# Kernel tuning notes

Hardware: AMD Instinct MI355X
Metric: run time of the kernel (lower is better)

## Reference

```python
import jax, jax.numpy as jnp
import numpy as np

B, D, L = 16, 256, 200
T = 1000   # max_frame_length
K = 3      # kernel_size
DW, DC = 4, 2


def setup_inputs() -> dict:
    key = jax.random.key(0)
    ks = jax.random.split(key, 16)
    plen = jax.random.randint(ks[0], (B,), 150, L + 1)
    pm = jnp.arange(L)[None, :] < plen[:, None]              # (B,L) True=valid
    phoneme_mask = pm[:, None, :]                            # (B,1,L)
    durations = jax.random.uniform(ks[1], (B, L), minval=1.0, maxval=8.0) * pm
    phoneme = jax.random.normal(ks[2], (B, D, L), dtype=jnp.float32)
    s = 0.05
    params = {
        'Wpw': jax.random.normal(ks[3], (D, D)) * s, 'bpw': jnp.zeros((D,)),
        'Cw': jax.random.normal(ks[4], (8, D, K)) * s, 'cbw': jnp.zeros((8,)),
        'Mw': jax.random.normal(ks[5], (10, DW)) * s, 'mbw': jnp.zeros((DW,)),
        'Lw': jax.random.normal(ks[6], (DW * D, D)) * s, 'lbw': jnp.zeros((D,)),
        'Wpc': jax.random.normal(ks[7], (D, D)) * s, 'bpc': jnp.zeros((D,)),
        'Cc': jax.random.normal(ks[8], (8, D, K)) * s, 'cbc': jnp.zeros((8,)),
        'Mc': jax.random.normal(ks[9], (10, DC)) * s, 'mbc': jnp.zeros((DC,)),
        'Lc': jax.random.normal(ks[10], (DW * DC, D)) * s, 'lbc': jnp.zeros((D,)),
        'Wo': jax.random.normal(ks[11], (D, 2 * D)) * s, 'bo': jnp.zeros((2 * D,)),
    }
    return {'durations': durations, 'phoneme': phoneme, 'phoneme_mask': phoneme_mask, **params}


def _conv_swish(x, W1, b1, Ck, cb, pm):
    # 1x1 conv (proj) then kernel-K 'same' conv then SiLU; mask padded phones
    h = jnp.einsum('od,bdl->bol', W1, x) + b1[None, :, None]
    h = jax.lax.conv_general_dilated(h, Ck, (1,), 'SAME',
                                     dimension_numbers=('NCH', 'OIH', 'NCH')) + cb[None, :, None]
    h = jax.nn.silu(h)
    h = jnp.where(pm[:, None, :], h, 0.0)
    return h.transpose(0, 2, 1)  # (B, L, 8)


def _mlp(S, E, h, M, mb):
    # concat start/end boundary scalars with per-phone conv features -> (B,T,L,10)
    feat = jnp.concatenate([S[..., None], E[..., None],
                            jnp.broadcast_to(h[:, None], (B, T, L, 8))], axis=-1)
    return jax.nn.silu(feat @ M + mb)


def _forward(durations, phoneme, phoneme_mask, Wpw, bpw, Cw, cbw, Mw, mbw, Lw, lbw,
             Wpc, bpc, Cc, cbc, Mc, mbc, Lc, lbc, Wo, bo):
    pm = phoneme_mask[:, 0, :]                                          # (B,L)
    frame_lengths = jnp.clip(jnp.round(durations.sum(-1)).astype(jnp.int32), 0, T)
    frame_mask = jnp.arange(T)[None, :] < frame_lengths[:, None]        # (B,T)
    attn_mask = frame_mask[:, :, None] & pm[:, None, :]                 # (B,T,L)
    sd = jnp.cumsum(durations, axis=-1)                                 # (B,L)
    sk = sd - durations
    t = jnp.arange(1, T + 1, dtype=durations.dtype)
    S = jnp.where(attn_mask, t[None, :, None] - sk[:, None, :], 0.0)    # (B,T,L)
    E = jnp.where(attn_mask, (sd - sk)[:, None, :], 0.0)                # (B,T,L)

    h_w = _conv_swish(phoneme, Wpw, bpw, Cw, cbw, pm)
    w = _mlp(S, E, h_w, Mw, mbw)                                        # (B,T,L,DW)
    w = jnp.where(pm[:, None, :, None], w, -jnp.inf)
    w = jax.nn.softmax(w, axis=2)                                       # softmax over phones
    w = jnp.where(frame_mask[:, :, None, None], w, 0.0)

    h_c = _conv_swish(phoneme, Wpc, bpc, Cc, cbc, pm)
    c = _mlp(S, E, h_c, Mc, mbc)                                        # (B,T,L,DC)

    wh = jnp.einsum('btlq,bdl->btqd', w, phoneme).reshape(B, T, DW * D) @ Lw + lbw
    wc = jnp.einsum('btlq,btlp->btqp', w, c).reshape(B, T, DW * DC) @ Lc + lbc
    whc = jnp.where(frame_mask[..., None], wh + wc, 0.0)                # (B,T,D)
    out = (whc @ Wo + bo).transpose(0, 2, 1)                            # (B,2D,T)
    return out, frame_mask, frame_lengths, w.transpose(0, 3, 1, 2)


def reference(durations, phoneme, phoneme_mask, Wpw, bpw, Cw, cbw, Mw, mbw, Lw, lbw,
              Wpc, bpc, Cc, cbc, Mc, mbc, Lc, lbc, Wo, bo):
    out, frame_mask, frame_lengths, w = _forward(
        durations, phoneme, phoneme_mask, Wpw, bpw, Cw, cbw, Mw, mbw, Lw, lbw,
        Wpc, bpc, Cc, cbc, Mc, mbc, Lc, lbc, Wo, bo)
    mean, log_std = jnp.split(out, 2, axis=1)                           # (B,D,T) each
    return (mean, log_std, frame_mask, frame_lengths, w)
```

## Files before the change

kernel.cpp:

```cpp
#include <hip/hip_runtime.h>
#include <hip/hip_bf16.h>
#include <math.h>

#define NB 16
#define ND 256
#define NL 200
#define NT 1000

typedef unsigned short ushort_t;
typedef __bf16 bf16x8 __attribute__((ext_vector_type(8)));
typedef float f32x4 __attribute__((ext_vector_type(4)));

#define OFF_PHT   0u
#define OFF_SK    4966400u
#define OFF_EW    4969600u
#define OFF_EC    4975744u
#define OFF_BW2   4981888u
#define OFF_BC2   4981912u
#define OFF_FL    4981936u
#define OFF_GT    11535552u
#define OFF_WOT   15221952u
#define OFF_BASE  15287488u
#define OFF_PHTB  15320256u
#define OFF_LWT   15844544u

__device__ __forceinline__ float silu_f(float x){ return x / (1.f + __expf(-x)); }
__device__ __forceinline__ ushort_t f2bf(float x){
  __hip_bfloat16 h = __float2bfloat16(x);
  return *(ushort_t*)&h;
}

__global__ __launch_bounds__(256) void k_stage1(
    const float* __restrict__ dur, const float* __restrict__ ph,
    const float* __restrict__ Wp_w, const float* __restrict__ C_w, const float* __restrict__ bp_w,
    const float* __restrict__ Wp_c, const float* __restrict__ C_c, const float* __restrict__ bp_c,
    const float* __restrict__ Wo, const float* __restrict__ Lw,
    float* __restrict__ sk_ws, int* __restrict__ fl_ws,
    float* __restrict__ o_fm, float* __restrict__ o_fl,
    float* __restrict__ Ew, float* __restrict__ Ec,
    float* __restrict__ bw2, float* __restrict__ bc2,
    ushort_t* __restrict__ WoT, ushort_t* __restrict__ LwT,
    float* __restrict__ phT, ushort_t* __restrict__ phTb)
{
  int bid = blockIdx.x, tid = threadIdx.x;
  if (bid < 16){
    int b = bid;
    __shared__ float sdur[NL];
    __shared__ float ssk[NL];
    __shared__ int sfl;
    if (tid < NL) sdur[tid] = dur[b*NL + tid];
    __syncthreads();
    if (tid == 0){
      float run = 0.f;
      for (int l = 0; l < NL; ++l){ ssk[l] = run; run += sdur[l]; }
      int fl = (int)rintf(run);
      fl = fl < 0 ? 0 : (fl > NT ? NT : fl);
      sfl = fl; fl_ws[b] = fl; o_fl[b] = (float)fl;
    }
    __syncthreads();
    if (tid < NL) sk_ws[b*NL + tid] = ssk[tid];
    for (int t = tid; t < NT; t += 256) o_fm[b*NT + t] = (t < sfl) ? 1.f : 0.f;
  } else if (bid < 1600){
    int sbid = bid - 16;
    if (sbid < 48){
      int gid = sbid*256 + tid;
      int branch = gid / 6144;
      int r = gid % 6144;
      int d = r & 255;
      int ock = r >> 8;
      int oc = ock / 3, k = ock % 3;
      const float* Wp = branch ? Wp_c : Wp_w;
      const float* C  = branch ? C_c  : C_w;
      float acc = 0.f;
      for (int i = 0; i < ND; ++i) acc += C[(oc*ND + i)*3 + k] * Wp[i*ND + d];
      (branch ? Ec : Ew)[r] = acc;
      if (d == 0){
        const float* bp = branch ? bp_c : bp_w;
        float bb = 0.f;
        for (int i = 0; i < ND; ++i) bb += C[(oc*ND + i)*3 + k] * bp[i];
        (branch ? bc2 : bw2)[ock] = bb;
      }
    } else {
      int gid = (sbid - 48)*256 + tid;
      if (gid < 131072){
        int n = gid >> 8, k = gid & 255;
        WoT[gid] = f2bf(Wo[(size_t)k*512 + n]);
      } else {
        int r = gid - 131072;
        int d = r & 255;
        int qn = r >> 8;
        int q = qn >> 8, n = qn & 255;
        LwT[r] = f2bf(Lw[((size_t)q*256 + d)*256 + n]);
      }
    }
  } else {
    int r = bid - 1600;
    int xb = r & 7, yb = (r >> 3) & 7, b = r >> 6;
    int l0 = xb*32, d0 = yb*32;
    int tx = tid & 31, ty = tid >> 5;
    __shared__ float tile[32][33];
    #pragma unroll
    for (int i = 0; i < 4; ++i){
      int d = d0 + ty + i*8, l = l0 + tx;
      tile[ty + i*8][tx] = (l < NL) ? ph[((size_t)b*ND + d)*NL + l] : 0.f;
    }
    __syncthreads();
    #pragma unroll
    for (int i = 0; i < 4; ++i){
      int l = l0 + ty + i*8, d = d0 + tx;
      float v = tile[tx][ty + i*8];
      if (l < NL) phT[((size_t)b*NL + l)*ND + d] = v;
      phTb[((size_t)b*256 + l)*ND + d] = f2bf(v);
    }
  }
}

__global__ __launch_bounds__(256) void k_stage2(
    const float* __restrict__ phT,
    const float* __restrict__ dur, const float* __restrict__ sk_ws,
    const float* __restrict__ Ew, const float* __restrict__ Ec,
    const float* __restrict__ bw2, const float* __restrict__ bc2,
    const float* __restrict__ cbw, const float* __restrict__ cbc,
    const float* __restrict__ Mw, const float* __restrict__ mbw,
    const float* __restrict__ Mc, const float* __restrict__ mbc,
    float4* __restrict__ base,
    const ushort_t* __restrict__ LwT, const ushort_t* __restrict__ phTb,
    ushort_t* __restrict__ Gt)
{
  __shared__ __align__(16) unsigned char smem[128*136*2];
  int bid = blockIdx.x, tid = threadIdx.x;
  if (bid < 256){
    int b = bid >> 4, x = bid & 15;
    if (x >= 13){
      int l0 = 208 + (x - 13)*16;
      if (tid < 32)
        base[((size_t)(b*256 + l0 + (tid >> 1)))*2 + (tid & 1)] = make_float4(0,0,0,0);
      return;
    }
    float (*sh)[17] = (float (*)[17])smem;
    int lu = tid >> 4, u = tid & 15;
    int l = x*16 + lu;
    float h = 0.f;
    if (l < NL){
      int branch = u >> 3, oc = u & 7;
      const float* E  = branch ? Ec  : Ew;
      const float* b2 = branch ? bc2 : bw2;
      float val = (branch ? cbc : cbw)[oc];
      #pragma unroll
      for (int k = 0; k < 3; ++k){
        int ll = l + k - 1;
        if (ll < 0 || ll >= NL) continue;
        float acc = b2[oc*3 + k];
        const float4* Er = (const float4*)(E + (oc*3 + k)*ND);
        const float4* pr = (const float4*)(phT + ((size_t)b*NL + ll)*ND);
        #pragma unroll 8
        for (int d = 0; d < 64; ++d){
          float4 e = Er[d], p = pr[d];
          acc += e.x*p.x + e.y*p.y + e.z*p.z + e.w*p.w;
        }
        val += acc;
      }
      float pm = (dur[b*NL + l] > 0.5f) ? 1.f : 0.f;
      h = silu_f(val) * pm;
    }
    sh[lu][u] = h;
    __syncthreads();
    if (tid < 16){
      int ll = x*16 + tid;
      float4 o0 = make_float4(0,0,0,0);
      float4 o1 = make_float4(0,0,0,0);
      if (ll < NL){
        float dl  = dur[b*NL + ll];
        float pm  = (dl > 0.5f) ? 1.f : 0.f;
        float skl = sk_ws[b*NL + ll];
        float c1[4], c2[2];
        #pragma unroll
        for (int q = 0; q < 4; ++q) c1[q] = mbw[q] + dl*Mw[4 + q] - skl*Mw[q];
        #pragma unroll
        for (int p = 0; p < 2; ++p) c2[p] = mbc[p] + dl*Mc[2 + p] - skl*Mc[p];
        #pragma unroll
        for (int j = 0; j < 8; ++j){
          float hwv = sh[tid][j], hcv = sh[tid][8 + j];
          #pragma unroll
          for (int q = 0; q < 4; ++q) c1[q] += hwv*Mw[(2 + j)*4 + q];
          #pragma unroll
          for (int p = 0; p < 2; ++p) c2[p] += hcv*Mc[(2 + j)*2 + p];
        }
        o0 = make_float4(c1[0], c1[1], c1[2], c1[3]);
        o1 = make_float4(c2[0], c2[1], pm, 0.f);
      }
      base[((size_t)(b*256 + ll))*2 + 0] = o0;
      base[((size_t)(b*256 + ll))*2 + 1] = o1;
    }
  } else {
    int r = bid - 256;
    int xb = r & 1, yb = (r >> 1) & 1, bq = r >> 2;
    int b = bq >> 2, q = bq & 3;
    int m0 = yb * 128;
    int n0 = xb * 128;
    int lane = tid & 63, wave = tid >> 6;
    int wm = wave >> 1, wn = wave & 1;
    int col = lane & 15, kg4 = lane >> 4;
    f32x4 acc[4][4] = {};
    for (int kt = 0; kt < 8; ++kt){
      int k0 = kt*32;
      bf16x8 afr[4], bfr[4];
      #pragma unroll
      for (int i = 0; i < 4; ++i)
        afr[i] = *(const bf16x8*)(LwT + ((size_t)(q*256 + m0 + wm*64 + i*16 + col))*256 + k0 + kg4*8);
      #pragma unroll
      for (int j = 0; j < 4; ++j)
        bfr[j] = *(const bf16x8*)(phTb + ((size_t)(b*256 + n0 + wn*64 + j*16 + col))*256 + k0 + kg4*8);
      #pragma unroll
      for (int i = 0; i < 4; ++i)
        #pragma unroll
        for (int j = 0; j < 4; ++j)
          acc[i][j] = __builtin_amdgcn_mfma_f32_16x16x32_bf16(afr[i], bfr[j], acc[i][j], 0, 0, 0);
    }
    ushort_t (*st2)[136] = (ushort_t (*)[136])smem;
    int rq = lane >> 4;
    #pragma unroll
    for (int i = 0; i < 4; ++i){
      #pragma unroll
      for (int rr = 0; rr < 4; ++rr){
        int rl = wm*64 + i*16 + rq*4 + rr;
        #pragma unroll
        for (int j = 0; j < 4; ++j){
          int cl = wn*64 + j*16 + col;
          st2[rl][cl] = f2bf(acc[i][j][rr]);
        }
      }
    }
    __syncthreads();
    #pragma unroll
    for (int rep = 0; rep < 8; ++rep){
      int row = rep*16 + (tid >> 4);
      int ch  = tid & 15;
      int l   = n0 + ch*8;
      if (l < NL){
        int n = m0 + row;
        *(uint4*)(Gt + ((size_t)(b*ND + n))*800 + q*NL + l) = *(const uint4*)&st2[row][ch*8];
      }
    }
  }
}

#define AP 808
__global__ __launch_bounds__(512, 4) void k_wv_fused(
    const float4* __restrict__ base,
    const int* __restrict__ fl_ws,
    const float* __restrict__ Mw, const float* __restrict__ Mc,
    const ushort_t* __restrict__ Gt,
    const float* __restrict__ Lc,
    const float* __restrict__ lbc,
    const float* __restrict__ lbw,
    const ushort_t* __restrict__ WoT,
    const float* __restrict__ bo,
    float* __restrict__ wout,
    float* __restrict__ o_mean, float* __restrict__ o_lstd)
{
  __shared__ ushort_t As[32*AP];
  __shared__ float    wcs[32][8];
  int b = blockIdx.x;
  int m0 = blockIdx.y * 32;
  int tid = threadIdx.x, lane = tid & 63, wave = tid >> 6;
  int col = lane & 15, kg4 = lane >> 4;
  int fl = fl_ws[b];

  for (int s = 0; s < 4; ++s){
    int tl = wave*4 + s;
    int t = m0 + tl;
    if (t >= fl){
      for (int k = lane; k < 800; k += 64) As[tl*AP + k] = 0;
      if (lane < 8) wcs[tl][lane] = 0.f;
      if (t < NT){
        float4 z4 = make_float4(0,0,0,0);
        #pragma unroll
        for (int q = 0; q < 4; ++q)
          if (lane < 50)
            *(float4*)&wout[(((size_t)(b*4 + q))*NT + t)*NL + lane*4] = z4;
      }
      continue;
    }
    float t1 = (float)(t + 1);
    float tqw[4], tqc[2];
    #pragma unroll
    for (int q = 0; q < 4; ++q) tqw[q] = t1 * Mw[q];
    #pragma unroll
    for (int p = 0; p < 2; ++p) tqc[p] = t1 * Mc[p];
    float z[4][4], cv[4][2], msk[4];
    float m[4] = {-INFINITY, -INFINITY, -INFINITY, -INFINITY};
    #pragma unroll
    for (int c = 0; c < 4; ++c){
      int l = c*64 + lane;
      float4 b0 = base[((size_t)(b*256 + l))*2 + 0];
      float4 b1 = base[((size_t)(b*256 + l))*2 + 1];
      float pm = b1.z;
      msk[c] = pm;
      float zz[4] = { b0.x + tqw[0], b0.y + tqw[1], b0.z + tqw[2], b0.w + tqw[3] };
      #pragma unroll
      for (int q = 0; q < 4; ++q){
        float sv = silu_f(zz[q]);
        z[c][q] = (pm > 0.f) ? sv : -INFINITY;
        m[q] = fmaxf(m[q], z[c][q]);
      }
      cv[c][0] = silu_f(b1.x + tqc[0]);
      cv[c][1] = silu_f(b1.y + tqc[1]);
    }
    #pragma unroll
    for (int q = 0; q < 4; ++q){
      float v = m[q];
      #pragma unroll
      for (int off = 32; off; off >>= 1) v = fmaxf(v, __shfl_xor(v, off));
      m[q] = v;
    }
    float s4[4] = {0,0,0,0};
    #pragma unroll
    for (int c = 0; c < 4; ++c){
      #pragma unroll
      for (int q = 0; q < 4; ++q){
        float e = (msk[c] > 0.f) ? __expf(z[c][q] - m[q]) : 0.f;
        z[c][q] = e;
        s4[q] += e;
      }
    }
    #pragma unroll
    for (int q = 0; q < 4; ++q){
      float v = s4[q];
      #pragma unroll
      for (int off = 32; off; off >>= 1) v += __shfl_xor(v, off);
      s4[q] = 1.f / v;
    }
    float wc[8] = {0,0,0,0,0,0,0,0};
    #pragma unroll
    for (int c = 0; c < 4; ++c){
      int l = c*64 + lane;
      bool lv = l < NL;
      #pragma unroll
      for (int q = 0; q < 4; ++q){
        float wq = z[c][q] * s4[q];
        if (lv){
          wout[(((size_t)(b*4 + q))*NT + t)*NL + l] = wq;
          As[tl*AP + q*NL + l] = f2bf(wq);
        }
        wc[q*2 + 0] += wq * cv[c][0];
        wc[q*2 + 1] += wq * cv[c][1];
      }
    }
    #pragma unroll
    for (int u = 0; u < 8; ++u){
      float v = wc[u];
      #pragma unroll
      for (int off = 32; off; off >>= 1) v += __shfl_xor(v, off);
      wc[u] = v;
    }
    if (lane == 0){
      #pragma unroll
      for (int u = 0; u < 8; ++u) wcs[tl][u] = wc[u];
    }
  }
  __syncthreads();

  f32x4 acc[2][2] = {};
  const ushort_t* Gb = Gt + (size_t)b*ND*800;
  for (int kt = 0; kt < 25; ++kt){
    int k0 = kt*32;
    bf16x8 afr[2], bfr[2];
    #pragma unroll
    for (int i = 0; i < 2; ++i)
      afr[i] = *(const bf16x8*)(&As[(i*16 + col)*AP + k0 + kg4*8]);
    #pragma unroll
    for (int j = 0; j < 2; ++j)
      bfr[j] = *(const bf16x8*)(Gb + ((size_t)(wave*32 + j*16 + col))*800 + k0 + kg4*8);
    #pragma unroll
    for (int i = 0; i < 2; ++i)
      #pragma unroll
      for (int j = 0; j < 2; ++j)
        acc[i][j] = __builtin_amdgcn_mfma_f32_16x16x32_bf16(afr[i], bfr[j], acc[i][j], 0, 0, 0);
  }
  __syncthreads();

  ushort_t (*stc)[264] = (ushort_t (*)[264])As;
  {
    int rq = lane >> 4;
    float lcn[2][8], lbn[2], lbwn[2];
    #pragma unroll
    for (int j = 0; j < 2; ++j){
      int n = wave*32 + j*16 + col;
      lbn[j] = lbc[n]; lbwn[j] = lbw[n];
      #pragma unroll
      for (int u = 0; u < 8; ++u) lcn[j][u] = Lc[u*ND + n];
    }
    #pragma unroll
    for (int i = 0; i < 2; ++i){
      #pragma unroll
      for (int r = 0; r < 4; ++r){
        int tl = i*16 + rq*4 + r;
        int t = m0 + tl;
        if (t >= NT) continue;
        float f = (t < fl) ? 1.f : 0.f;
        #pragma unroll
        for (int j = 0; j < 2; ++j){
          float vcv = lbn[j]
            + wcs[tl][0]*lcn[j][0] + wcs[tl][1]*lcn[j][1]
            + wcs[tl][2]*lcn[j][2] + wcs[tl][3]*lcn[j][3]
            + wcs[tl][4]*lcn[j][4] + wcs[tl][5]*lcn[j][5]
            + wcs[tl][6]*lcn[j][6] + wcs[tl][7]*lcn[j][7];
          int n = wave*32 + j*16 + col;
          stc[tl][n] = f2bf(f * (acc[i][j][r] + lbwn[j] + vcv));
        }
      }
    }
  }
  __syncthreads();

  {
    f32x4 acc2[4][2] = {};
    for (int kt = 0; kt < 8; ++kt){
      int k0 = kt*32;
      bf16x8 afr[4], bfr[2];
      #pragma unroll
      for (int j = 0; j < 2; ++j)
        bfr[j] = *(const bf16x8*)(&stc[j*16 + col][k0 + kg4*8]);
      #pragma unroll
      for (int i = 0; i < 4; ++i)
        afr[i] = *(const bf16x8*)(WoT + ((size_t)(wave*64 + i*16 + col))*ND + k0 + kg4*8);
      #pragma unroll
      for (int i = 0; i < 4; ++i)
        #pragma unroll
        for (int j = 0; j < 2; ++j)
          acc2[i][j] = __builtin_amdgcn_mfma_f32_16x16x32_bf16(afr[i], bfr[j], acc2[i][j], 0, 0, 0);
    }
    int rq = lane >> 4;
    #pragma unroll
    for (int i = 0; i < 4; ++i){
      #pragma unroll
      for (int r = 0; r < 4; ++r){
        int s = wave*64 + i*16 + rq*4 + r;
        float bov = bo[s];
        #pragma unroll
        for (int j = 0; j < 2; ++j){
          int t = m0 + j*16 + col;
          if (t >= NT) continue;
          float v = acc2[i][j][r] + bov;
          if (s < ND) o_mean[((size_t)b*ND + s)*NT + t] = v;
          else        o_lstd[((size_t)b*ND + (s - ND))*NT + t] = v;
        }
      }
    }
  }
}

extern "C" void kernel_launch(void* const* d_in, const int* in_sizes, int n_in,
                              void* d_out, int out_size, void* d_ws, size_t ws_size,
                              hipStream_t stream)
{
  const float* dur = (const float*)d_in[0];
  const float* ph  = (const float*)d_in[1];
  const float* Wpw = (const float*)d_in[3];
  const float* bpw = (const float*)d_in[4];
  const float* Cw  = (const float*)d_in[5];
  const float* cbw = (const float*)d_in[6];
  const float* Mw  = (const float*)d_in[7];
  const float* mbw = (const float*)d_in[8];
  const float* Lw  = (const float*)d_in[9];
  const float* lbw = (const float*)d_in[10];
  const float* Wpc = (const float*)d_in[11];
  const float* bpc = (const float*)d_in[12];
  const float* Cc  = (const float*)d_in[13];
  const float* cbc = (const float*)d_in[14];
  const float* Mc  = (const float*)d_in[15];
  const float* mbc = (const float*)d_in[16];
  const float* Lc  = (const float*)d_in[17];
  const float* lbc = (const float*)d_in[18];
  const float* Wo  = (const float*)d_in[19];
  const float* bo  = (const float*)d_in[20];

  float* out    = (float*)d_out;
  float* o_mean = out;
  float* o_lstd = out + (size_t)NB*ND*NT;
  float* o_fm   = o_lstd + (size_t)NB*ND*NT;
  float* o_fl   = o_fm + NB*NT;
  float* o_w    = o_fl + NB;

  float* ws   = (float*)d_ws;
  float* phT  = ws + OFF_PHT;
  float* sk   = ws + OFF_SK;
  float* Ew   = ws + OFF_EW;
  float* Ec   = ws + OFF_EC;
  float* bw2  = ws + OFF_BW2;
  float* bc2  = ws + OFF_BC2;
  int*   fl   = (int*)(ws + OFF_FL);
  ushort_t* Gt   = (ushort_t*)(ws + OFF_GT);
  ushort_t* WoT  = (ushort_t*)(ws + OFF_WOT);
  float4*   base = (float4*)(ws + OFF_BASE);
  ushort_t* phTb = (ushort_t*)(ws + OFF_PHTB);
  ushort_t* LwT  = (ushort_t*)(ws + OFF_LWT);

  k_stage1<<<2624, 256, 0, stream>>>(dur, ph, Wpw, Cw, bpw, Wpc, Cc, bpc, Wo, Lw,
                                     sk, fl, o_fm, o_fl, Ew, Ec, bw2, bc2,
                                     WoT, LwT, phT, phTb);
  k_stage2<<<512, 256, 0, stream>>>(phT, dur, sk, Ew, Ec, bw2, bc2, cbw, cbc,
                                    Mw, mbw, Mc, mbc, base, LwT, phTb, Gt);
  {
    dim3 g(NB, 32);
    k_wv_fused<<<g, 512, 0, stream>>>(base, fl, Mw, Mc, Gt, Lc, lbc, lbw,
                                      WoT, bo, o_w, o_mean, o_lstd);
  }
}
```

Before: 239.3 us.

## Double frame tile to 64 with 1024-thread blocks and early-exit padded tiles

The fused weighting/projection kernel now handles 64 frames per block with 16 waves, so each Gt and WoT fragment loaded from global memory is reused across twice as many frames. The per-wave MFMA tiling is reshaped to match. Blocks whose whole tile lies past the frame length skip all compute and only write zeros to the attention output and bias to the mean/log_std outputs. The cost is LDS use roughly doubling per block to about 100KB, fewer blocks in flight, and a 1024-thread launch bound.

```diff
diff --git a/kernel.cpp b/kernel.cpp
--- a/kernel.cpp
+++ b/kernel.cpp
@@ -246,7 +246,8 @@
 }
 
 #define AP 808
-__global__ __launch_bounds__(512, 4) void k_wv_fused(
+#define TT 64
+__global__ __launch_bounds__(1024, 4) void k_wv_fused(
     const float4* __restrict__ base,
     const int* __restrict__ fl_ws,
     const float* __restrict__ Mw, const float* __restrict__ Mc,
@@ -259,13 +260,35 @@
     float* __restrict__ wout,
     float* __restrict__ o_mean, float* __restrict__ o_lstd)
 {
-  __shared__ ushort_t As[32*AP];
-  __shared__ float    wcs[32][8];
+  __shared__ ushort_t As[TT*AP];
+  __shared__ float    wcs[TT][8];
   int b = blockIdx.x;
-  int m0 = blockIdx.y * 32;
+  int m0 = blockIdx.y * TT;
   int tid = threadIdx.x, lane = tid & 63, wave = tid >> 6;
   int col = lane & 15, kg4 = lane >> 4;
   int fl = fl_ws[b];
+
+  if (fl <= m0){
+    for (int idx = tid; idx < TT*4*50; idx += 1024){
+      int tl = idx / 200;
+      int rqs = idx - tl*200;
+      int q = rqs / 50, seg = rqs - q*50;
+      int t = m0 + tl;
+      if (t < NT)
+        *(float4*)&wout[(((size_t)(b*4 + q))*NT + t)*NL + seg*4] = make_float4(0,0,0,0);
+    }
+    for (int idx = tid; idx < 512*16; idx += 1024){
+      int s = idx >> 4, j = idx & 15;
+      int t0 = m0 + j*4;
+      if (t0 + 3 < NT){
+        float v = bo[s];
+        float4 v4 = make_float4(v, v, v, v);
+        if (s < ND) *(float4*)&o_mean[((size_t)b*ND + s)*NT + t0] = v4;
+        else        *(float4*)&o_lstd[((size_t)b*ND + (s - ND))*NT + t0] = v4;
+      }
+    }
+    return;
+  }
 
   for (int s = 0; s < 4; ++s){
     int tl = wave*4 + s;
@@ -361,53 +384,43 @@
   }
   __syncthreads();
 
-  f32x4 acc[2][2] = {};
+  f32x4 acc[4] = {};
   const ushort_t* Gb = Gt + (size_t)b*ND*800;
   for (int kt = 0; kt < 25; ++kt){
     int k0 = kt*32;
-    bf16x8 afr[2], bfr[2];
-    #pragma unroll
-    for (int i = 0; i < 2; ++i)
+    bf16x8 afr[4], bfr;
+    #pragma unroll
+    for (int i = 0; i < 4; ++i)
       afr[i] = *(const bf16x8*)(&As[(i*16 + col)*AP + k0 + kg4*8]);
-    #pragma unroll
-    for (int j = 0; j < 2; ++j)
-      bfr[j] = *(const bf16x8*)(Gb + ((size_t)(wave*32 + j*16 + col))*800 + k0 + kg4*8);
-    #pragma unroll
-    for (int i = 0; i < 2; ++i)
-      #pragma unroll
-      for (int j = 0; j < 2; ++j)
-        acc[i][j] = __builtin_amdgcn_mfma_f32_16x16x32_bf16(afr[i], bfr[j], acc[i][j], 0, 0, 0);
+    bfr = *(const bf16x8*)(Gb + ((size_t)(wave*16 + col))*800 + k0 + kg4*8);
+    #pragma unroll
+    for (int i = 0; i < 4; ++i)
+      acc[i] = __builtin_amdgcn_mfma_f32_16x16x32_bf16(afr[i], bfr, acc[i], 0, 0, 0);
   }
   __syncthreads();
 
   ushort_t (*stc)[264] = (ushort_t (*)[264])As;
   {
     int rq = lane >> 4;
-    float lcn[2][8], lbn[2], lbwn[2];
-    #pragma unroll
-    for (int j = 0; j < 2; ++j){
-      int n = wave*32 + j*16 + col;
-      lbn[j] = lbc[n]; lbwn[j] = lbw[n];
-      #pragma unroll
-      for (int u = 0; u < 8; ++u) lcn[j][u] = Lc[u*ND + n];
-    }
-    #pragma unroll
-    for (int i = 0; i < 2; ++i){
+    int n = wave*16 + col;
+    float lbn = lbc[n], lbwn = lbw[n];
+    float lcn[8];
+    #pragma unroll
+    for (int u = 0; u < 8; ++u) lcn[u] = Lc[u*ND + n];
+    #pragma unroll
+    for (int i = 0; i < 4; ++i){
       #pragma unroll
       for (int r = 0; r < 4; ++r){
         int tl = i*16 + rq*4 + r;
         int t = m0 + tl;
-        if (t >= NT) continue;
-        float f = (t < fl) ? 1.f : 0.f;
-        #pragma unroll
-        for (int j = 0; j < 2; ++j){
-          float vcv = lbn[j]
-            + wcs[tl][0]*lcn[j][0] + wcs[tl][1]*lcn[j][1]
-            + wcs[tl][2]*lcn[j][2] + wcs[tl][3]*lcn[j][3]
-            + wcs[tl][4]*lcn[j][4] + wcs[tl][5]*lcn[j][5]
-            + wcs[tl][6]*lcn[j][6] + wcs[tl][7]*lcn[j][7];
-          int n = wave*32 + j*16 + col;
-          stc[tl][n] = f2bf(f * (acc[i][j][r] + lbwn[j] + vcv));
+        if (t < NT){
+          float f = (t < fl) ? 1.f : 0.f;
+          float vcv = lbn
+            + wcs[tl][0]*lcn[0] + wcs[tl][1]*lcn[1]
+            + wcs[tl][2]*lcn[2] + wcs[tl][3]*lcn[3]
+            + wcs[tl][4]*lcn[4] + wcs[tl][5]*lcn[5]
+            + wcs[tl][6]*lcn[6] + wcs[tl][7]*lcn[7];
+          stc[tl][n] = f2bf(f * (acc[i][r] + lbwn + vcv));
         }
       }
     }
@@ -415,36 +428,37 @@
   __syncthreads();
 
   {
-    f32x4 acc2[4][2] = {};
+    f32x4 acc2[2][4] = {};
     for (int kt = 0; kt < 8; ++kt){
       int k0 = kt*32;
-      bf16x8 afr[4], bfr[2];
-      #pragma unroll
-      for (int j = 0; j < 2; ++j)
+      bf16x8 afr[2], bfr[4];
+      #pragma unroll
+      for (int j = 0; j < 4; ++j)
         bfr[j] = *(const bf16x8*)(&stc[j*16 + col][k0 + kg4*8]);
       #pragma unroll
-      for (int i = 0; i < 4; ++i)
-        afr[i] = *(const bf16x8*)(WoT + ((size_t)(wave*64 + i*16 + col))*ND + k0 + kg4*8);
-      #pragma unroll
-      for (int i = 0; i < 4; ++i)
-        #pragma unroll
-        for (int j = 0; j < 2; ++j)
+      for (int i = 0; i < 2; ++i)
+        afr[i] = *(const bf16x8*)(WoT + ((size_t)(wave*32 + i*16 + col))*ND + k0 + kg4*8);
+      #pragma unroll
+      for (int i = 0; i < 2; ++i)
+        #pragma unroll
+        for (int j = 0; j < 4; ++j)
           acc2[i][j] = __builtin_amdgcn_mfma_f32_16x16x32_bf16(afr[i], bfr[j], acc2[i][j], 0, 0, 0);
     }
     int rq = lane >> 4;
     #pragma unroll
-    for (int i = 0; i < 4; ++i){
+    for (int i = 0; i < 2; ++i){
       #pragma unroll
       for (int r = 0; r < 4; ++r){
-        int s = wave*64 + i*16 + rq*4 + r;
+        int s = wave*32 + i*16 + rq*4 + r;
         float bov = bo[s];
         #pragma unroll
-        for (int j = 0; j < 2; ++j){
+        for (int j = 0; j < 4; ++j){
           int t = m0 + j*16 + col;
-          if (t >= NT) continue;
-          float v = acc2[i][j][r] + bov;
-          if (s < ND) o_mean[((size_t)b*ND + s)*NT + t] = v;
-          else        o_lstd[((size_t)b*ND + (s - ND))*NT + t] = v;
+          if (t < NT){
+            float v = acc2[i][j][r] + bov;
+            if (s < ND) o_mean[((size_t)b*ND + s)*NT + t] = v;
+            else        o_lstd[((size_t)b*ND + (s - ND))*NT + t] = v;
+          }
         }
       }
     }
@@ -503,8 +517,8 @@
   k_stage2<<<512, 256, 0, stream>>>(phT, dur, sk, Ew, Ec, bw2, bc2, cbw, cbc,
                                     Mw, mbw, Mc, mbc, base, LwT, phTb, Gt);
   {
-    dim3 g(NB, 32);
-    k_wv_fused<<<g, 512, 0, stream>>>(base, fl, Mw, Mc, Gt, Lc, lbc, lbw,
-                                      WoT, bo, o_w, o_mean, o_lstd);
+    dim3 g(NB, 16);
+    k_wv_fused<<<g, 1024, 0, stream>>>(base, fl, Mw, Mc, Gt, Lc, lbc, lbw,
+                                       WoT, bo, o_w, o_mean, o_lstd);
   }
 }
```

Result: faster. 234.5 us (-2.0%).
